# Kernel optimization log

Hardware: AMD Instinct MI355X
Metric: run time of the kernel (lower is better)

## Reference

```python
import jax, jax.numpy as jnp
import numpy as np

N = 100_000      # total nodes (entities + relations)
D = 128          # embed_dim
E_ER = 1_000_000 # entity->relation edges
E_EE = 500_000   # entity->entity edges


def setup_inputs() -> dict:
    key = jax.random.key(0)
    ks = jax.random.split(key, 14)
    s = 0.05
    return {
        "node_emb": jax.random.normal(ks[0], (N, D), jnp.float32),
        "er_src": jax.random.randint(ks[1], (E_ER,), 0, N),
        "er_dst": jax.random.randint(ks[2], (E_ER,), 0, N),
        "ee_src": jax.random.randint(ks[3], (E_EE,), 0, N),
        "ee_dst": jax.random.randint(ks[4], (E_EE,), 0, N),
        "ee_weight": jax.random.uniform(ks[5], (E_EE,), jnp.float32),
        # learned params (stored as (in, out) so y = x @ W + b)
        "W_attn_w": jax.random.normal(ks[6], (2 * D, D), jnp.float32) * s,
        "W_attn_b": jax.random.normal(ks[7], (D,), jnp.float32) * s,
        "w0_w": jax.random.normal(ks[8], (D,), jnp.float32) * s,
        "w0_b": jax.random.normal(ks[9], (), jnp.float32) * s,
        "W_self_w": jax.random.normal(ks[10], (D, D), jnp.float32) * s,
        "W_self_b": jax.random.normal(ks[11], (D,), jnp.float32) * s,
        "W_neigh_w": jax.random.normal(ks[12], (D, D), jnp.float32) * s,
        "W_neigh_b": jax.random.normal(ks[13], (D,), jnp.float32) * s,
    }


def _segment_softmax(values, seg_ids, num_segments):
    # torch scatter_reduce_ starts from zeros with include_self=True -> max includes 0
    seg_max = jnp.maximum(
        jax.ops.segment_max(values, seg_ids, num_segments=num_segments), 0.0)
    exp_v = jnp.exp(values - seg_max[seg_ids])
    seg_sum = jax.ops.segment_sum(exp_v, seg_ids, num_segments=num_segments)
    return exp_v / (seg_sum[seg_ids] + 1e-9)


def reference(node_emb, er_src, er_dst, ee_src, ee_dst, ee_weight,
              W_attn_w, W_attn_b, w0_w, w0_b, W_self_w, W_self_b,
              W_neigh_w, W_neigh_b):
    n = node_emb.shape[0]
    # --- entity -> relation attention messages ---
    h_emb = node_emb[er_src]                      # (E, D)
    r_emb = node_emb[er_dst]                      # (E, D)
    pair = jnp.concatenate([r_emb, h_emb], axis=-1)  # (E, 2D)
    e_ij = jnp.tanh(pair @ W_attn_w + W_attn_b) @ w0_w + w0_b  # (E,)
    attn = _segment_softmax(e_ij, er_src, n)      # (E,)
    r_msg = r_emb @ W_neigh_w + W_neigh_b         # (E, D)
    agg = jnp.zeros_like(node_emb).at[er_src].add(attn[:, None] * r_msg)
    # --- entity -> entity weighted messages (note: scatter index is ee_src, as in source) ---
    src_emb = node_emb[ee_src]                    # (E2, D)
    ee_msg = src_emb @ W_neigh_w + W_neigh_b
    agg = agg.at[ee_src].add(ee_weight[:, None] * ee_msg)
    # --- self update ---
    return jnp.tanh(node_emb @ W_self_w + W_self_b + agg)
```

## Files before the change

### kernel.cpp

```cpp
#include <hip/hip_runtime.h>

#define DD 128

typedef short s16x8 __attribute__((ext_vector_type(8)));
typedef float f32x4 __attribute__((ext_vector_type(4)));

__device__ __forceinline__ float tanh_fast(float x) {
  float e = __expf(2.0f * x);
  return 1.0f - 2.0f / (e + 1.0f);
}

__device__ __forceinline__ unsigned short f2bf(float f) {
  unsigned u = __float_as_uint(f);
  u += 0x7FFFu + ((u >> 16) & 1u);
  return (unsigned short)(u >> 16);
}

__device__ __forceinline__ float bf2f(unsigned short u) {
  return __uint_as_float(((unsigned)u) << 16);
}

__device__ __forceinline__ float bfu(unsigned w, int odd) {
  return __uint_as_float(odd ? (w & 0xFFFF0000u) : (w << 16));
}

extern "C" __global__ __launch_bounds__(256) void k_prep(
    const float* __restrict__ emb, unsigned short* __restrict__ ebf, int total8,
    int nb_tobf, const float* __restrict__ Wattn, unsigned short* __restrict__ WB,
    const float* __restrict__ Wself, const float* __restrict__ Wneigh,
    unsigned short* __restrict__ WBh, unsigned short* __restrict__ WBl) {
  const int b = blockIdx.x;
  const int tid = threadIdx.x;
  if (b < nb_tobf) {
    int i = b * 256 + tid;
    if (i >= total8) return;
    const float4* e4 = (const float4*)emb;
    float4 x = e4[(size_t)i * 2];
    float4 y = e4[(size_t)i * 2 + 1];
    uint4 o;
    o.x = (unsigned)f2bf(x.x) | ((unsigned)f2bf(x.y) << 16);
    o.y = (unsigned)f2bf(x.z) | ((unsigned)f2bf(x.w) << 16);
    o.z = (unsigned)f2bf(y.x) | ((unsigned)f2bf(y.y) << 16);
    o.w = (unsigned)f2bf(y.z) | ((unsigned)f2bf(y.w) << 16);
    *(uint4*)(ebf + (size_t)i * 8) = o;
  } else if (b < nb_tobf + 16) {
    int t = (b - nb_tobf) * 256 + tid;
    int lane = t & 63;
    int cks = t >> 6;
    int ks = cks & 3, ct = cks >> 2;
    int c = ct * 16 + (lane & 15);
    int kb = ks * 32 + ((lane >> 4) << 3);
    const float* srcp = (c < DD) ? (Wattn + (size_t)kb * DD + c)
                                 : (Wattn + (size_t)(DD + kb) * DD + (c - DD));
    unsigned short* dst = WB + (size_t)t * 8;
#pragma unroll
    for (int j = 0; j < 8; ++j) dst[j] = f2bf(srcp[(size_t)j * DD]);
  } else {
    int t = (b - nb_tobf - 16) * 256 + tid;
    int lane = t & 63;
    int cks = t >> 6;
    int ks = cks & 7, ct = cks >> 3;
    int c = ct * 16 + (lane & 15);
    int k0 = ks * 32 + ((lane >> 4) << 3);
#pragma unroll
    for (int j = 0; j < 8; ++j) {
      int k = k0 + j;
      float v = (k < DD) ? Wself[(size_t)k * DD + c]
                         : Wneigh[(size_t)(k - DD) * DD + c];
      unsigned short h = f2bf(v);
      float r = v - bf2f(h);
      WBh[(size_t)t * 8 + j] = h;
      WBl[(size_t)t * 8 + j] = f2bf(r);
    }
  }
}

extern "C" __global__ __launch_bounds__(256) void k_edges(
    const int* __restrict__ er_src, int* __restrict__ count, int nER, int hb,
    const int* __restrict__ ee_src, const float* __restrict__ ee_w,
    float* __restrict__ g, int nEE) {
  const int b = blockIdx.x;
  if (b < hb) {
    int e = b * 256 + threadIdx.x;
    if (e < nER) atomicAdd(&count[er_src[e]], 1);
  } else {
    int e = (b - hb) * 256 + threadIdx.x;
    if (e < nEE) unsafeAtomicAdd(&g[ee_src[e]], ee_w[e]);
  }
}

extern "C" __global__ __launch_bounds__(256) void k_pq_mfma(
    const unsigned short* __restrict__ ebf, const unsigned short* __restrict__ WB,
    const float* __restrict__ battn, unsigned short* __restrict__ PQ, int n) {
  const int wave = threadIdx.x >> 6, lane = threadIdx.x & 63;
  const int v0 = blockIdx.x * 64 + wave * 16;
  const int row = v0 + (lane & 15);
  const int kb = (lane >> 4) << 3;
  const bool rok = row < n;
  const s16x8 zf = {0, 0, 0, 0, 0, 0, 0, 0};
  s16x8 a[4];
#pragma unroll
  for (int ks = 0; ks < 4; ++ks)
    a[ks] = rok ? *(const s16x8*)(ebf + (size_t)row * DD + ks * 32 + kb) : zf;
  f32x4 acc[16];
#pragma unroll
  for (int ct = 0; ct < 16; ++ct) acc[ct] = (f32x4)(0.f);
  const s16x8* wb = (const s16x8*)WB;
#pragma unroll
  for (int ct = 0; ct < 16; ++ct) {
#pragma unroll
    for (int ks = 0; ks < 4; ++ks) {
      s16x8 b = wb[(ct * 4 + ks) * 64 + lane];
      acc[ct] = __builtin_amdgcn_mfma_f32_16x16x32_bf16(a[ks], b, acc[ct], 0, 0, 0);
    }
  }
  const int r0 = (lane >> 4) << 2;
  const int col0 = lane & 15;
#pragma unroll
  for (int ct = 0; ct < 16; ++ct) {
    int c = ct * 16 + col0;
    float bias = (c < DD) ? battn[c] : 0.f;
#pragma unroll
    for (int r = 0; r < 4; ++r) {
      int v = v0 + r0 + r;
      if (v < n) PQ[(size_t)v * 256 + c] = f2bf(acc[ct][r] + bias);
    }
  }
}

extern "C" __global__ __launch_bounds__(256) void k_scan(
    const int* __restrict__ in, int* __restrict__ outp,
    int* __restrict__ bsum, int n) {
  __shared__ int s[512];
  __shared__ int total;
  const int t = threadIdx.x;
  const int base = blockIdx.x * 512;
  for (int i = t; i < 512; i += 256) s[i] = (base + i < n) ? in[base + i] : 0;
  __syncthreads();
  for (int d = 1; d < 512; d <<= 1) {
    int stride = d * 2;
    int nidx = 512 / stride;
    if (t < nidx) {
      int idx = (t + 1) * stride - 1;
      s[idx] += s[idx - d];
    }
    __syncthreads();
  }
  if (t == 0) { total = s[511]; s[511] = 0; }
  __syncthreads();
  for (int d = 256; d >= 1; d >>= 1) {
    int stride = d * 2;
    int nidx = 512 / stride;
    if (t < nidx) {
      int idx = (t + 1) * stride - 1;
      int tmp = s[idx - d];
      s[idx - d] = s[idx];
      s[idx] += tmp;
    }
    __syncthreads();
  }
  for (int i = t; i < 512; i += 256)
    if (base + i < n) outp[base + i] = s[i];
  if (t == 0) bsum[blockIdx.x] = total;
}

extern "C" __global__ __launch_bounds__(256) void k_scan_add(
    int* __restrict__ off, int* __restrict__ off_mut,
    const int* __restrict__ bofs, int n, int total) {
  int base = blockIdx.x * 512;
  int add = bofs[blockIdx.x];
  for (int i = threadIdx.x; i < 512; i += 256) {
    int idx = base + i;
    if (idx < n) {
      int val = off[idx] + add;
      off[idx] = val;
      off_mut[idx] = val;
    }
  }
  if (blockIdx.x == 0 && threadIdx.x == 0) off[n] = total;
}

extern "C" __global__ __launch_bounds__(256) void k_scatter_dst(
    const int* __restrict__ src, const int* __restrict__ dstp,
    int* __restrict__ off_mut, int* __restrict__ dst_s, int nE) {
  int e = blockIdx.x * 256 + threadIdx.x;
  if (e >= nE) return;
  int pos = atomicAdd(&off_mut[src[e]], 1);
  dst_s[pos] = dstp[e];
}

__device__ __forceinline__ void proc_edge(
    uint4 pv, uint4 ev, const float q[8], const float w[8], float wb,
    float a[8], float& ssv) {
  unsigned pw[4] = {pv.x, pv.y, pv.z, pv.w};
  unsigned ew[4] = {ev.x, ev.y, ev.z, ev.w};
  float part = 0.f;
#pragma unroll
  for (int j = 0; j < 8; ++j) {
    float x = bfu(pw[j >> 1], j & 1) + q[j];
    part = fmaf(tanh_fast(x), w[j], part);
  }
  part += __shfl_xor(part, 8);
  part += __shfl_xor(part, 4);
  part += __shfl_xor(part, 2);
  part += __shfl_xor(part, 1);
  float p = __expf(part + wb);
  ssv += p;
#pragma unroll
  for (int j = 0; j < 8; ++j)
    a[j] = fmaf(p, bfu(ew[j >> 1], j & 1), a[j]);
}

extern "C" __global__ __launch_bounds__(256) void k_fused(
    const unsigned short* __restrict__ PQ, const unsigned short* __restrict__ ebf,
    const int* __restrict__ off, const int* __restrict__ dst_s,
    const float* __restrict__ w0w, const float* __restrict__ w0b,
    float* __restrict__ U, float* __restrict__ ssum, int n) {
  int v = (blockIdx.x * 256 + threadIdx.x) >> 6;
  int lane = threadIdx.x & 63;
  if (v >= n) return;
  const int l16 = lane & 15;
  const int grp = lane >> 4;
  const int start = off[v], end = off[v + 1];
  float q[8], w[8];
  {
    uint4 qv = *(const uint4*)(PQ + (size_t)v * 256 + DD + l16 * 8);
    unsigned qq[4] = {qv.x, qv.y, qv.z, qv.w};
    float4 wa = *(const float4*)&w0w[l16 * 8];
    float4 wc = *(const float4*)&w0w[l16 * 8 + 4];
    w[0] = wa.x; w[1] = wa.y; w[2] = wa.z; w[3] = wa.w;
    w[4] = wc.x; w[5] = wc.y; w[6] = wc.z; w[7] = wc.w;
#pragma unroll
    for (int j = 0; j < 8; ++j) q[j] = bfu(qq[j >> 1], j & 1);
  }
  const float wb = w0b[0];
  float a[8] = {0.f, 0.f, 0.f, 0.f, 0.f, 0.f, 0.f, 0.f};
  float ssv = 0.f;
  int i = start + grp;
  for (; i + 4 < end; i += 8) {
    int d0 = dst_s[i];
    int d1 = dst_s[i + 4];
    uint4 pv0 = *(const uint4*)(PQ + (size_t)d0 * 256 + l16 * 8);
    uint4 ev0 = *(const uint4*)(ebf + (size_t)d0 * DD + l16 * 8);
    uint4 pv1 = *(const uint4*)(PQ + (size_t)d1 * 256 + l16 * 8);
    uint4 ev1 = *(const uint4*)(ebf + (size_t)d1 * DD + l16 * 8);
    proc_edge(pv0, ev0, q, w, wb, a, ssv);
    proc_edge(pv1, ev1, q, w, wb, a, ssv);
  }
  if (i < end) {
    int d0 = dst_s[i];
    uint4 pv0 = *(const uint4*)(PQ + (size_t)d0 * 256 + l16 * 8);
    uint4 ev0 = *(const uint4*)(ebf + (size_t)d0 * DD + l16 * 8);
    proc_edge(pv0, ev0, q, w, wb, a, ssv);
  }
#pragma unroll
  for (int j = 0; j < 8; ++j) {
    a[j] += __shfl_xor(a[j], 16);
    a[j] += __shfl_xor(a[j], 32);
  }
  ssv += __shfl_xor(ssv, 16);
  ssv += __shfl_xor(ssv, 32);
  if (grp == 0) {
    float4 o0 = make_float4(a[0], a[1], a[2], a[3]);
    float4 o1 = make_float4(a[4], a[5], a[6], a[7]);
    *(float4*)(U + (size_t)v * DD + l16 * 8) = o0;
    *(float4*)(U + (size_t)v * DD + l16 * 8 + 4) = o1;
    if (l16 == 0) ssum[v] = ssv;
  }
}

extern "C" __global__ __launch_bounds__(256) void k_out_mfma(
    const float* __restrict__ emb, const float* __restrict__ U,
    const float* __restrict__ ssum, const float* __restrict__ g,
    const unsigned short* __restrict__ WBh, const unsigned short* __restrict__ WBl,
    const float* __restrict__ bself, const float* __restrict__ bneigh,
    float* __restrict__ out, int n) {
  const int wave = threadIdx.x >> 6, lane = threadIdx.x & 63;
  const int v0 = blockIdx.x * 64 + wave * 16;
  const int row = v0 + (lane & 15);
  const int kb = (lane >> 4) << 3;
  const bool rok = row < n;
  float inv = 0.f, gv = 0.f;
  if (rok) {
    float sv = ssum[row];
    inv = 1.f / (sv + 1e-9f);
    gv = g[row];
  }
  s16x8 ah[8], al[8];
#pragma unroll
  for (int ks = 0; ks < 8; ++ks) {
    int k0 = (ks & 3) * 32 + kb;
    float x[8] = {0.f, 0.f, 0.f, 0.f, 0.f, 0.f, 0.f, 0.f};
    if (rok) {
      float4 ea = *(const float4*)(emb + (size_t)row * DD + k0);
      float4 eb = *(const float4*)(emb + (size_t)row * DD + k0 + 4);
      x[0] = ea.x; x[1] = ea.y; x[2] = ea.z; x[3] = ea.w;
      x[4] = eb.x; x[5] = eb.y; x[6] = eb.z; x[7] = eb.w;
      if (ks >= 4) {
        float4 ua = *(const float4*)(U + (size_t)row * DD + k0);
        float4 ub = *(const float4*)(U + (size_t)row * DD + k0 + 4);
        x[0] = fmaf(gv, x[0], ua.x * inv);
        x[1] = fmaf(gv, x[1], ua.y * inv);
        x[2] = fmaf(gv, x[2], ua.z * inv);
        x[3] = fmaf(gv, x[3], ua.w * inv);
        x[4] = fmaf(gv, x[4], ub.x * inv);
        x[5] = fmaf(gv, x[5], ub.y * inv);
        x[6] = fmaf(gv, x[6], ub.z * inv);
        x[7] = fmaf(gv, x[7], ub.w * inv);
      }
    }
    unsigned short hh[8], ll[8];
#pragma unroll
    for (int j = 0; j < 8; ++j) {
      unsigned short h = f2bf(x[j]);
      hh[j] = h;
      ll[j] = f2bf(x[j] - bf2f(h));
    }
    ah[ks] = *(const s16x8*)hh;
    al[ks] = *(const s16x8*)ll;
  }
  f32x4 acc[8];
#pragma unroll
  for (int ct = 0; ct < 8; ++ct) acc[ct] = (f32x4)(0.f);
  const s16x8* wbh = (const s16x8*)WBh;
  const s16x8* wbl = (const s16x8*)WBl;
#pragma unroll
  for (int ct = 0; ct < 8; ++ct) {
#pragma unroll
    for (int ks = 0; ks < 8; ++ks) {
      s16x8 bh = wbh[(ct * 8 + ks) * 64 + lane];
      s16x8 bl = wbl[(ct * 8 + ks) * 64 + lane];
      acc[ct] = __builtin_amdgcn_mfma_f32_16x16x32_bf16(ah[ks], bh, acc[ct], 0, 0, 0);
      acc[ct] = __builtin_amdgcn_mfma_f32_16x16x32_bf16(al[ks], bh, acc[ct], 0, 0, 0);
      acc[ct] = __builtin_amdgcn_mfma_f32_16x16x32_bf16(ah[ks], bl, acc[ct], 0, 0, 0);
    }
  }
  const int r0 = (lane >> 4) << 2;
  const int col0 = lane & 15;
  float tgr[4];
#pragma unroll
  for (int r = 0; r < 4; ++r) {
    int v = v0 + r0 + r;
    float tg = 0.f;
    if (v < n) {
      float sv = ssum[v];
      tg = sv / (sv + 1e-9f) + g[v];
    }
    tgr[r] = tg;
  }
#pragma unroll
  for (int ct = 0; ct < 8; ++ct) {
    int c = ct * 16 + col0;
    float bs = bself[c], bn = bneigh[c];
#pragma unroll
    for (int r = 0; r < 4; ++r) {
      int v = v0 + r0 + r;
      if (v < n) out[(size_t)v * DD + c] = tanh_fast(acc[ct][r] + bs + tgr[r] * bn);
    }
  }
}

static inline size_t al16(size_t x) { return (x + 15) & ~(size_t)15; }

extern "C" void kernel_launch(void* const* d_in, const int* in_sizes, int n_in,
                              void* d_out, int out_size, void* d_ws, size_t ws_size,
                              hipStream_t stream) {
  const float* emb = (const float*)d_in[0];
  const int* er_src = (const int*)d_in[1];
  const int* er_dst = (const int*)d_in[2];
  const int* ee_src = (const int*)d_in[3];
  const float* ee_w = (const float*)d_in[5];
  const float* Wattn = (const float*)d_in[6];
  const float* battn = (const float*)d_in[7];
  const float* w0w = (const float*)d_in[8];
  const float* w0b = (const float*)d_in[9];
  const float* Wself = (const float*)d_in[10];
  const float* bself = (const float*)d_in[11];
  const float* Wneigh = (const float*)d_in[12];
  const float* bneigh = (const float*)d_in[13];
  const int n = in_sizes[0] / DD;
  const int nER = in_sizes[1];
  const int nEE = in_sizes[3];

  char* w = (char*)d_ws;
  size_t o = 0;
  unsigned short* ebf = (unsigned short*)(w + o); o += al16((size_t)n * DD * 2);
  unsigned short* PQ  = (unsigned short*)(w + o); o += al16((size_t)n * 256 * 2);
  float* U = (float*)(w + o);   o += al16((size_t)n * DD * 4);
  int* dst_s = (int*)(w + o);   o += al16((size_t)nER * 4);
  int* count = (int*)(w + o);   o += al16((size_t)n * 4);
  float* g = (float*)(w + o);   o += al16((size_t)n * 4);
  int* off = (int*)(w + o);     o += al16((size_t)(n + 4) * 4);
  int* off_mut = (int*)(w + o); o += al16((size_t)n * 4);
  float* ssum = (float*)(w + o); o += al16((size_t)n * 4);
  unsigned short* WB = (unsigned short*)(w + o);   o += 65536;
  unsigned short* WB2h = (unsigned short*)(w + o); o += 65536;
  unsigned short* WB2l = (unsigned short*)(w + o); o += 65536;
  int* bsum = (int*)(w + o);    o += 4096;
  int* dummy = (int*)(w + o);   o += 64;

  const int nb = (n + 511) / 512;
  const int total8 = n * DD / 8;
  const int nb_tobf = (total8 + 255) / 256;
  const int hb = (nER + 255) / 256;
  const int db = (nEE + 255) / 256;

  hipMemsetAsync(count, 0, (size_t)n * 8, stream);

  k_prep<<<nb_tobf + 32, 256, 0, stream>>>(emb, ebf, total8, nb_tobf, Wattn, WB,
                                           Wself, Wneigh, WB2h, WB2l);
  k_edges<<<hb + db, 256, 0, stream>>>(er_src, count, nER, hb, ee_src, ee_w, g,
                                       nEE);
  k_pq_mfma<<<(n + 63) / 64, 256, 0, stream>>>(ebf, WB, battn, PQ, n);
  k_scan<<<nb, 256, 0, stream>>>(count, off, bsum, n);
  k_scan<<<1, 256, 0, stream>>>(bsum, bsum, dummy, nb);
  k_scan_add<<<nb, 256, 0, stream>>>(off, off_mut, bsum, n, nER);
  k_scatter_dst<<<(nER + 255) / 256, 256, 0, stream>>>(er_src, er_dst, off_mut,
                                                       dst_s, nER);
  k_fused<<<(n + 3) / 4, 256, 0, stream>>>(PQ, ebf, off, dst_s, w0w, w0b,
                                           U, ssum, n);
  k_out_mfma<<<(n + 63) / 64, 256, 0, stream>>>(emb, U, ssum, g, WB2h, WB2l,
                                                bself, bneigh, (float*)d_out, n);
}
```

Measured before the change: 406.9 us.

## Interleave P and bf16 embedding rows into one PQE buffer, fold conversion into GEMM

Drops the separate fp32-to-bf16 embedding pass and has the PQ GEMM kernel convert on load, writing the bf16 embedding into a combined 384-wide row layout [P | emb | Q]. The per-edge gather in the fused kernel then reads P and the embedding from one contiguous 768-byte row instead of two separate arrays, which should improve locality for the random gathers. The edge loop is simplified from a 2-way unroll to a single edge per iteration, and tanh uses a hardware reciprocal plus an FMA. The single-edge loop may expose more load latency, and the rcp approximation slightly changes precision.

```diff
diff --git a/kernel.cpp b/kernel.cpp
--- a/kernel.cpp
+++ b/kernel.cpp
@@ -7,7 +7,8 @@
 
 __device__ __forceinline__ float tanh_fast(float x) {
   float e = __expf(2.0f * x);
-  return 1.0f - 2.0f / (e + 1.0f);
+  float r = __builtin_amdgcn_rcpf(e + 1.0f);
+  return fmaf(-2.0f, r, 1.0f);
 }
 
 __device__ __forceinline__ unsigned short f2bf(float f) {
@@ -25,26 +26,13 @@
 }
 
 extern "C" __global__ __launch_bounds__(256) void k_prep(
-    const float* __restrict__ emb, unsigned short* __restrict__ ebf, int total8,
-    int nb_tobf, const float* __restrict__ Wattn, unsigned short* __restrict__ WB,
+    const float* __restrict__ Wattn, unsigned short* __restrict__ WB,
     const float* __restrict__ Wself, const float* __restrict__ Wneigh,
     unsigned short* __restrict__ WBh, unsigned short* __restrict__ WBl) {
   const int b = blockIdx.x;
   const int tid = threadIdx.x;
-  if (b < nb_tobf) {
-    int i = b * 256 + tid;
-    if (i >= total8) return;
-    const float4* e4 = (const float4*)emb;
-    float4 x = e4[(size_t)i * 2];
-    float4 y = e4[(size_t)i * 2 + 1];
-    uint4 o;
-    o.x = (unsigned)f2bf(x.x) | ((unsigned)f2bf(x.y) << 16);
-    o.y = (unsigned)f2bf(x.z) | ((unsigned)f2bf(x.w) << 16);
-    o.z = (unsigned)f2bf(y.x) | ((unsigned)f2bf(y.y) << 16);
-    o.w = (unsigned)f2bf(y.z) | ((unsigned)f2bf(y.w) << 16);
-    *(uint4*)(ebf + (size_t)i * 8) = o;
-  } else if (b < nb_tobf + 16) {
-    int t = (b - nb_tobf) * 256 + tid;
+  if (b < 16) {
+    int t = b * 256 + tid;
     int lane = t & 63;
     int cks = t >> 6;
     int ks = cks & 3, ct = cks >> 2;
@@ -56,7 +44,7 @@
 #pragma unroll
     for (int j = 0; j < 8; ++j) dst[j] = f2bf(srcp[(size_t)j * DD]);
   } else {
-    int t = (b - nb_tobf - 16) * 256 + tid;
+    int t = (b - 16) * 256 + tid;
     int lane = t & 63;
     int cks = t >> 6;
     int ks = cks & 7, ct = cks >> 3;
@@ -90,18 +78,29 @@
 }
 
 extern "C" __global__ __launch_bounds__(256) void k_pq_mfma(
-    const unsigned short* __restrict__ ebf, const unsigned short* __restrict__ WB,
-    const float* __restrict__ battn, unsigned short* __restrict__ PQ, int n) {
+    const float* __restrict__ emb, const unsigned short* __restrict__ WB,
+    const float* __restrict__ battn, unsigned short* __restrict__ PQE, int n) {
   const int wave = threadIdx.x >> 6, lane = threadIdx.x & 63;
   const int v0 = blockIdx.x * 64 + wave * 16;
   const int row = v0 + (lane & 15);
   const int kb = (lane >> 4) << 3;
   const bool rok = row < n;
-  const s16x8 zf = {0, 0, 0, 0, 0, 0, 0, 0};
   s16x8 a[4];
 #pragma unroll
-  for (int ks = 0; ks < 4; ++ks)
-    a[ks] = rok ? *(const s16x8*)(ebf + (size_t)row * DD + ks * 32 + kb) : zf;
+  for (int ks = 0; ks < 4; ++ks) {
+    unsigned short tmp[8] = {0, 0, 0, 0, 0, 0, 0, 0};
+    if (rok) {
+      float4 xa = *(const float4*)(emb + (size_t)row * DD + ks * 32 + kb);
+      float4 xb = *(const float4*)(emb + (size_t)row * DD + ks * 32 + kb + 4);
+      tmp[0] = f2bf(xa.x); tmp[1] = f2bf(xa.y);
+      tmp[2] = f2bf(xa.z); tmp[3] = f2bf(xa.w);
+      tmp[4] = f2bf(xb.x); tmp[5] = f2bf(xb.y);
+      tmp[6] = f2bf(xb.z); tmp[7] = f2bf(xb.w);
+    }
+    a[ks] = *(const s16x8*)tmp;
+    if (rok)
+      *(s16x8*)(PQE + (size_t)row * 384 + 128 + ks * 32 + kb) = a[ks];
+  }
   f32x4 acc[16];
 #pragma unroll
   for (int ct = 0; ct < 16; ++ct) acc[ct] = (f32x4)(0.f);
@@ -120,10 +119,11 @@
   for (int ct = 0; ct < 16; ++ct) {
     int c = ct * 16 + col0;
     float bias = (c < DD) ? battn[c] : 0.f;
+    int dsto = (c < DD) ? c : (c - DD + 256);
 #pragma unroll
     for (int r = 0; r < 4; ++r) {
       int v = v0 + r0 + r;
-      if (v < n) PQ[(size_t)v * 256 + c] = f2bf(acc[ct][r] + bias);
+      if (v < n) PQE[(size_t)v * 384 + dsto] = f2bf(acc[ct][r] + bias);
     }
   }
 }
@@ -189,33 +189,11 @@
   dst_s[pos] = dstp[e];
 }
 
-__device__ __forceinline__ void proc_edge(
-    uint4 pv, uint4 ev, const float q[8], const float w[8], float wb,
-    float a[8], float& ssv) {
-  unsigned pw[4] = {pv.x, pv.y, pv.z, pv.w};
-  unsigned ew[4] = {ev.x, ev.y, ev.z, ev.w};
-  float part = 0.f;
-#pragma unroll
-  for (int j = 0; j < 8; ++j) {
-    float x = bfu(pw[j >> 1], j & 1) + q[j];
-    part = fmaf(tanh_fast(x), w[j], part);
-  }
-  part += __shfl_xor(part, 8);
-  part += __shfl_xor(part, 4);
-  part += __shfl_xor(part, 2);
-  part += __shfl_xor(part, 1);
-  float p = __expf(part + wb);
-  ssv += p;
-#pragma unroll
-  for (int j = 0; j < 8; ++j)
-    a[j] = fmaf(p, bfu(ew[j >> 1], j & 1), a[j]);
-}
-
 extern "C" __global__ __launch_bounds__(256) void k_fused(
-    const unsigned short* __restrict__ PQ, const unsigned short* __restrict__ ebf,
-    const int* __restrict__ off, const int* __restrict__ dst_s,
-    const float* __restrict__ w0w, const float* __restrict__ w0b,
-    float* __restrict__ U, float* __restrict__ ssum, int n) {
+    const unsigned short* __restrict__ PQE, const int* __restrict__ off,
+    const int* __restrict__ dst_s, const float* __restrict__ w0w,
+    const float* __restrict__ w0b, float* __restrict__ U,
+    float* __restrict__ ssum, int n) {
   int v = (blockIdx.x * 256 + threadIdx.x) >> 6;
   int lane = threadIdx.x & 63;
   if (v >= n) return;
@@ -224,7 +202,7 @@
   const int start = off[v], end = off[v + 1];
   float q[8], w[8];
   {
-    uint4 qv = *(const uint4*)(PQ + (size_t)v * 256 + DD + l16 * 8);
+    uint4 qv = *(const uint4*)(PQE + (size_t)v * 384 + 256 + l16 * 8);
     unsigned qq[4] = {qv.x, qv.y, qv.z, qv.w};
     float4 wa = *(const float4*)&w0w[l16 * 8];
     float4 wc = *(const float4*)&w0w[l16 * 8 + 4];
@@ -236,22 +214,28 @@
   const float wb = w0b[0];
   float a[8] = {0.f, 0.f, 0.f, 0.f, 0.f, 0.f, 0.f, 0.f};
   float ssv = 0.f;
-  int i = start + grp;
-  for (; i + 4 < end; i += 8) {
-    int d0 = dst_s[i];
-    int d1 = dst_s[i + 4];
-    uint4 pv0 = *(const uint4*)(PQ + (size_t)d0 * 256 + l16 * 8);
-    uint4 ev0 = *(const uint4*)(ebf + (size_t)d0 * DD + l16 * 8);
-    uint4 pv1 = *(const uint4*)(PQ + (size_t)d1 * 256 + l16 * 8);
-    uint4 ev1 = *(const uint4*)(ebf + (size_t)d1 * DD + l16 * 8);
-    proc_edge(pv0, ev0, q, w, wb, a, ssv);
-    proc_edge(pv1, ev1, q, w, wb, a, ssv);
-  }
-  if (i < end) {
-    int d0 = dst_s[i];
-    uint4 pv0 = *(const uint4*)(PQ + (size_t)d0 * 256 + l16 * 8);
-    uint4 ev0 = *(const uint4*)(ebf + (size_t)d0 * DD + l16 * 8);
-    proc_edge(pv0, ev0, q, w, wb, a, ssv);
+  for (int i = start + grp; i < end; i += 4) {
+    int d = dst_s[i];
+    const unsigned short* pe = PQE + (size_t)d * 384 + l16 * 8;
+    uint4 pv = *(const uint4*)pe;
+    uint4 ev = *(const uint4*)(pe + 128);
+    unsigned pw[4] = {pv.x, pv.y, pv.z, pv.w};
+    unsigned ew[4] = {ev.x, ev.y, ev.z, ev.w};
+    float part = 0.f;
+#pragma unroll
+    for (int j = 0; j < 8; ++j) {
+      float x = bfu(pw[j >> 1], j & 1) + q[j];
+      part = fmaf(tanh_fast(x), w[j], part);
+    }
+    part += __shfl_xor(part, 8);
+    part += __shfl_xor(part, 4);
+    part += __shfl_xor(part, 2);
+    part += __shfl_xor(part, 1);
+    float p = __expf(part + wb);
+    ssv += p;
+#pragma unroll
+    for (int j = 0; j < 8; ++j)
+      a[j] = fmaf(p, bfu(ew[j >> 1], j & 1), a[j]);
   }
 #pragma unroll
   for (int j = 0; j < 8; ++j) {
@@ -384,8 +368,7 @@
 
   char* w = (char*)d_ws;
   size_t o = 0;
-  unsigned short* ebf = (unsigned short*)(w + o); o += al16((size_t)n * DD * 2);
-  unsigned short* PQ  = (unsigned short*)(w + o); o += al16((size_t)n * 256 * 2);
+  unsigned short* PQE = (unsigned short*)(w + o); o += al16((size_t)n * 384 * 2);
   float* U = (float*)(w + o);   o += al16((size_t)n * DD * 4);
   int* dst_s = (int*)(w + o);   o += al16((size_t)nER * 4);
   int* count = (int*)(w + o);   o += al16((size_t)n * 4);
@@ -400,24 +383,21 @@
   int* dummy = (int*)(w + o);   o += 64;
 
   const int nb = (n + 511) / 512;
-  const int total8 = n * DD / 8;
-  const int nb_tobf = (total8 + 255) / 256;
   const int hb = (nER + 255) / 256;
   const int db = (nEE + 255) / 256;
 
   hipMemsetAsync(count, 0, (size_t)n * 8, stream);
 
-  k_prep<<<nb_tobf + 32, 256, 0, stream>>>(emb, ebf, total8, nb_tobf, Wattn, WB,
-                                           Wself, Wneigh, WB2h, WB2l);
+  k_prep<<<32, 256, 0, stream>>>(Wattn, WB, Wself, Wneigh, WB2h, WB2l);
+  k_pq_mfma<<<(n + 63) / 64, 256, 0, stream>>>(emb, WB, battn, PQE, n);
   k_edges<<<hb + db, 256, 0, stream>>>(er_src, count, nER, hb, ee_src, ee_w, g,
                                        nEE);
-  k_pq_mfma<<<(n + 63) / 64, 256, 0, stream>>>(ebf, WB, battn, PQ, n);
   k_scan<<<nb, 256, 0, stream>>>(count, off, bsum, n);
   k_scan<<<1, 256, 0, stream>>>(bsum, bsum, dummy, nb);
   k_scan_add<<<nb, 256, 0, stream>>>(off, off_mut, bsum, n, nER);
   k_scatter_dst<<<(nER + 255) / 256, 256, 0, stream>>>(er_src, er_dst, off_mut,
                                                        dst_s, nER);
-  k_fused<<<(n + 3) / 4, 256, 0, stream>>>(PQ, ebf, off, dst_s, w0w, w0b,
+  k_fused<<<(n + 3) / 4, 256, 0, stream>>>(PQE, off, dst_s, w0w, w0b,
                                            U, ssum, n);
   k_out_mfma<<<(n + 63) / 64, 256, 0, stream>>>(emb, U, ssum, g, WB2h, WB2l,
                                                 bself, bneigh, (float*)d_out, n);
```

After: 362.5 us. -10.9%, faster.
